# Optimization experiments

Hardware: AMD Instinct MI355X
Metric: run time of the kernel (lower is better)

Reference implementation:

```python
import jax, jax.numpy as jnp
import numpy as np

EPS = 1e-5

def layernorm(x, w, b):
    mu = x.mean(-1, keepdims=True)
    var = x.var(-1, keepdims=True)
    return (x - mu) / jnp.sqrt(var + EPS) * w + b

def silu(x):
    return x * jax.nn.sigmoid(x)

def causal_dwconv(x, w, b):
    # x: (B,L,D), w: (D,K) depthwise causal conv along L
    K = w.shape[1]
    xt = jnp.moveaxis(x, 1, 2)                      # (B,D,L)
    xt = jnp.pad(xt, ((0, 0), (0, 0), (K - 1, 0)))
    y = jax.lax.conv_general_dilated(xt, w[:, None, :], (1,), 'VALID',
        dimension_numbers=('NCH', 'OIH', 'NCH'), feature_group_count=w.shape[0])
    return jnp.moveaxis(y + b[None, :, None], 2, 1)

def mamba_layer(x, p):
    # LayerNorm + Mamba selective scan; returns (out, C) with C the per-step C projection ("C_fast")
    xn = layernorm(x, p['ln_w'], p['ln_b'])
    xz = xn @ p['in_proj_w']                        # (B,L,2*Di)
    Di = p['conv_w'].shape[0]
    xh, z = xz[..., :Di], xz[..., Di:]
    xh = silu(causal_dwconv(xh, p['conv_w'], p['conv_b']))
    dbl = xh @ p['x_proj_w']                        # (B,L,R+2*S)
    R = p['dt_proj_w'].shape[0]
    S = p['A_log'].shape[1]
    dt = jax.nn.softplus(dbl[..., :R] @ p['dt_proj_w'] + p['dt_proj_b'])  # (B,L,Di)
    Bm = dbl[..., R:R + S]                          # (B,L,S)
    Cm = dbl[..., R + S:]                           # (B,L,S)
    A = -jnp.exp(p['A_log'])                        # (Di,S)
    dA = jnp.exp(dt[..., None] * A)                 # (B,L,Di,S)
    dBx = dt[..., None] * Bm[:, :, None, :] * xh[..., None]
    def step(h, inp):
        a, bx = inp
        h = a * h + bx
        return h, h
    h0 = jnp.zeros((x.shape[0], Di, S), x.dtype)
    _, hs = jax.lax.scan(step, h0, (jnp.moveaxis(dA, 1, 0), jnp.moveaxis(dBx, 1, 0)))
    y = jnp.einsum('lbds,bls->bld', hs, Cm) + p['D'] * xh
    y = y * silu(z)
    return y @ p['out_proj_w'], Cm

def run_chunks(x, k, p):
    # contiguous L-chunks folded into batch (chunks are independent sequences)
    B, L, D = x.shape
    y, C = mamba_layer(x.reshape(B * k, L // k, D), p)
    return y.reshape(B, L, D), C.reshape(B, k, L // k, -1)

def batchnorm(h, g, b):
    mu = h.mean((0, 1))
    var = h.var((0, 1))
    return (h - mu) / jnp.sqrt(var + EPS) * g + b

def freq_ffn(x, fc1_w, bn1_g, bn1_b, r_mat, i_mat, rb, ib, fc2_w, bn2_g, bn2_b):
    h = jax.nn.relu(batchnorm(jnp.einsum('bnc,hc->bnh', x, fc1_w), bn1_g, bn1_b))
    xf = jnp.fft.fft(h, axis=1, norm='ortho')
    # torch einsum 'bnc,cc->bnc' multiplies by the DIAGONAL of the matrix
    rd = jnp.diagonal(r_mat)
    idg = jnp.diagonal(i_mat)
    xr = jax.nn.relu(xf.real * rd - xf.imag * idg + rb)
    xi = jax.nn.relu(xf.imag * rd + xf.real * idg + ib)
    h = jnp.fft.ifft(xr + 1j * xi, axis=1, norm='ortho').real.astype(x.dtype)
    return batchnorm(jnp.einsum('bnh,ch->bnc', h, fc2_w), bn2_g, bn2_b)


def setup_inputs() -> dict:
    key = jax.random.key(0)
    B, L, D = 4, 512, 128
    Di, S, R, K, H = 256, 64, 8, 4, 256
    ks = jax.random.split(key, 16)
    rn = lambda k, sh, s=1.0: (jax.random.normal(k, sh) * s).astype(jnp.float32)
    return {
        'x': rn(ks[0], (B, L, D)),
        'ln_w': jnp.ones((D,), jnp.float32), 'ln_b': jnp.zeros((D,), jnp.float32),
        'in_proj_w': rn(ks[1], (D, 2 * Di), D ** -0.5),
        'conv_w': rn(ks[2], (Di, K), 0.3),
        'conv_b': jnp.zeros((Di,), jnp.float32),
        'x_proj_w': rn(ks[3], (Di, R + 2 * S), Di ** -0.5),
        'dt_proj_w': rn(ks[4], (R, Di), R ** -0.5),
        'dt_proj_b': rn(ks[5], (Di,), 0.1) - 4.0,
        'A_log': jnp.log(jnp.tile(jnp.arange(1, S + 1, dtype=jnp.float32), (Di, 1))),
        'D_param': jnp.ones((Di,), jnp.float32),
        'out_proj_w': rn(ks[6], (Di, D), Di ** -0.5),
        'norm1_w': jnp.ones((D,), jnp.float32), 'norm1_b': jnp.zeros((D,), jnp.float32),
        'norm2_w': jnp.ones((D,), jnp.float32), 'norm2_b': jnp.zeros((D,), jnp.float32),
        'fc1_w': rn(ks[7], (H, D), D ** -0.5),
        'bn1_g': jnp.ones((H,), jnp.float32), 'bn1_b': jnp.zeros((H,), jnp.float32),
        'r_mat': rn(ks[8], (H, H), 0.02),
        'i_mat': rn(ks[9], (H, H), 0.02),
        'rb': rn(ks[10], (H,), 0.02),
        'ib': rn(ks[11], (H,), 0.02),
        'fc2_w': rn(ks[12], (D, H), H ** -0.5),
        'bn2_g': jnp.ones((D,), jnp.float32), 'bn2_b': jnp.zeros((D,), jnp.float32),
    }


def reference(x, ln_w, ln_b, in_proj_w, conv_w, conv_b, x_proj_w, dt_proj_w, dt_proj_b,
              A_log, D_param, out_proj_w, norm1_w, norm1_b, norm2_w, norm2_b,
              fc1_w, bn1_g, bn1_b, r_mat, i_mat, rb, ib, fc2_w, bn2_g, bn2_b):
    p = dict(ln_w=ln_w, ln_b=ln_b, in_proj_w=in_proj_w, conv_w=conv_w, conv_b=conv_b,
             x_proj_w=x_proj_w, dt_proj_w=dt_proj_w, dt_proj_b=dt_proj_b,
             A_log=A_log, D=D_param, out_proj_w=out_proj_w)
    x_o, C0 = mamba_layer(x, p)                 # full sequence
    y1, C1 = run_chunks(x, 2, p)                # 2 halves
    y2, C2 = run_chunks(x, 4, p)                # 4 quarters
    y3, C3 = run_chunks(x, 8, p)                # 8 eighths
    x_o = x_o + y1 + y2 + y3                    # drop_path = Identity
    xo = x + layernorm(x_o, norm1_w, norm1_b)
    out = xo + freq_ffn(layernorm(xo, norm2_w, norm2_b),
                        fc1_w, bn1_g, bn1_b, r_mat, i_mat, rb, ib, fc2_w, bn2_g, bn2_b)
    return out, C0, C1, C2, C3
```

## Files before the change

### kernel.cpp

```cpp
#include <hip/hip_runtime.h>
#include <hip/hip_bf16.h>
#include <math.h>


constexpr int NT = 2048;
constexpr int Di = 256;
constexpr float EPSF = 1e-5f;
constexpr float LOG2E = 1.4426950408889634f;
constexpr float ISQ512 = 0.04419417382415922f;

typedef __attribute__((ext_vector_type(8))) short short8;
typedef __attribute__((ext_vector_type(4))) float f32x4;

constexpr long O_COS   = 0;
constexpr long O_CS2B  = 512;
constexpr long O_CSIB  = 262656;
constexpr long O_A2    = 524800;
constexpr long O_FC1B  = 541184;
constexpr long O_FC2B  = 557568;
constexpr long O_RD    = 573952;
constexpr long O_IDG   = 574208;
constexpr long O_XN    = 574464;
constexpr long O_XZ    = 836608;
constexpr long O_XH    = 1885184;
constexpr long O_DBL   = 3982336;
constexpr long O_DTT   = 5096448;
constexpr long O_YS    = 7193600;
constexpr long O_YACC  = 9290752;
constexpr long O_XO1   = 9815040;
constexpr long O_XO    = 10077184;
constexpr long O_LN2B  = 10339328;
constexpr long O_H1    = 10404864;
constexpr long O_H1NTB = 10929152;
constexpr long O_XRI   = 11191296;
constexpr long O_XRITB = 12239872;
constexpr long O_H2B   = 12764160;
constexpr long O_F2    = 13026304;
constexpr long O_ST1   = 13288448;
constexpr long O_ST2   = 13288960;
constexpr long O_DXT   = O_H1;

__device__ __forceinline__ ushort bf16bits(float v) {
  __hip_bfloat16 h = __float2bfloat16(v);
  return *(ushort*)&h;
}

__global__ void k_costab(float* __restrict__ ws) {
  int m = threadIdx.x;
  ws[O_COS + m]       = cosf((float)m * (6.283185307179586f / 512.0f)) * ISQ512;
  ws[O_COS + m + 256] = cosf((float)(m + 256) * (6.283185307179586f / 512.0f)) * ISQ512;
}

__global__ void k_tables(const float* __restrict__ A_log,
                         const float* __restrict__ fc1_w,
                         const float* __restrict__ fc2_w,
                         const float* __restrict__ r_mat,
                         const float* __restrict__ i_mat,
                         float* __restrict__ ws) {
  const float* ct = ws + O_COS;
  __hip_bfloat16* cs2b = (__hip_bfloat16*)(ws + O_CS2B);
  __hip_bfloat16* csib = (__hip_bfloat16*)(ws + O_CSIB);
  int i = blockIdx.x * 256 + threadIdx.x;
  if (i < 524288) {
    int r = i >> 9, n = i & 511;
    float v;
    if (r < 512) v = ct[(r * n) & 511];
    else         v = -ct[((r - 512) * n + 384) & 511];
    cs2b[i] = __float2bfloat16(v);
  } else {
    int j = i - 524288;
    int n = j >> 10, kp = j & 1023;
    float v;
    if (kp < 512) v = ct[(n * kp) & 511];
    else          v = -ct[(n * (kp - 512) + 384) & 511];
    csib[j] = __float2bfloat16(v);
  }
  if (i < 16384) ws[O_A2 + i] = -expf(A_log[i]) * LOG2E;
  if (i < 32768) {
    ((__hip_bfloat16*)(ws + O_FC1B))[i] = __float2bfloat16(fc1_w[i]);
    ((__hip_bfloat16*)(ws + O_FC2B))[i] = __float2bfloat16(fc2_w[i]);
  }
  if (i < 256) {
    ws[O_RD + i] = r_mat[i * 256 + i];
    ws[O_IDG + i] = i_mat[i * 256 + i];
  }
}

__global__ void k_ln1(const float* __restrict__ x, const float* __restrict__ w,
                      const float* __restrict__ b, float* __restrict__ out) {
  int lane = threadIdx.x & 63;
  int t = (blockIdx.x * 256 + threadIdx.x) >> 6;
  float v0 = x[t * 128 + lane], v1 = x[t * 128 + 64 + lane];
  float s = v0 + v1, sq = v0 * v0 + v1 * v1;
#pragma unroll
  for (int off = 32; off; off >>= 1) { s += __shfl_xor(s, off); sq += __shfl_xor(sq, off); }
  float mu = s * (1.f / 128.f);
  float rstd = rsqrtf(sq * (1.f / 128.f) - mu * mu + EPSF);
  out[t * 128 + lane]      = (v0 - mu) * rstd * w[lane] + b[lane];
  out[t * 128 + 64 + lane] = (v1 - mu) * rstd * w[64 + lane] + b[64 + lane];
}

__global__ void k_lndbl(const float* __restrict__ x, const float* __restrict__ xo1,
                        const float* __restrict__ w1, const float* __restrict__ b1,
                        const float* __restrict__ w2, const float* __restrict__ b2,
                        float* __restrict__ xo, __hip_bfloat16* __restrict__ ln2b) {
  int lane = threadIdx.x & 63;
  int t = (blockIdx.x * 256 + threadIdx.x) >> 6;
  float u0 = xo1[t * 128 + lane], u1 = xo1[t * 128 + 64 + lane];
  float s = u0 + u1, sq = u0 * u0 + u1 * u1;
#pragma unroll
  for (int off = 32; off; off >>= 1) { s += __shfl_xor(s, off); sq += __shfl_xor(sq, off); }
  float mu = s * (1.f / 128.f);
  float rstd = rsqrtf(sq * (1.f / 128.f) - mu * mu + EPSF);
  float a0 = x[t * 128 + lane]      + (u0 - mu) * rstd * w1[lane] + b1[lane];
  float a1 = x[t * 128 + 64 + lane] + (u1 - mu) * rstd * w1[64 + lane] + b1[64 + lane];
  xo[t * 128 + lane] = a0;
  xo[t * 128 + 64 + lane] = a1;
  s = a0 + a1; sq = a0 * a0 + a1 * a1;
#pragma unroll
  for (int off = 32; off; off >>= 1) { s += __shfl_xor(s, off); sq += __shfl_xor(sq, off); }
  mu = s * (1.f / 128.f);
  rstd = rsqrtf(sq * (1.f / 128.f) - mu * mu + EPSF);
  ln2b[t * 128 + lane]      = __float2bfloat16((a0 - mu) * rstd * w2[lane] + b2[lane]);
  ln2b[t * 128 + 64 + lane] = __float2bfloat16((a1 - mu) * rstd * w2[64 + lane] + b2[64 + lane]);
}

__global__ __launch_bounds__(256) void k_gemm(const float* __restrict__ A,
                                              const float* __restrict__ B,
                                              float* __restrict__ C,
                                              int M, int N, int K,
                                              long sA, long sB, long sC) {
  A += (long)blockIdx.z * sA;
  B += (long)blockIdx.z * sB;
  C += (long)blockIdx.z * sC;
  __shared__ float As[16][68];
  __shared__ float Bs[16][68];
  int tid = threadIdx.x;
  int m0 = blockIdx.y * 64, n0 = blockIdx.x * 64;
  int arow = tid >> 2, ak4 = (tid & 3) * 4;
  int bkrow = tid >> 4, bn4 = (tid & 15) * 4;
  int tr = (tid >> 4) * 4, tc = (tid & 15) * 4;
  float acc[4][4] = {};
  for (int k0 = 0; k0 < K; k0 += 16) {
    float4 av = *(const float4*)&A[(long)(m0 + arow) * K + k0 + ak4];
    float4 bv = make_float4(0.f, 0.f, 0.f, 0.f);
    if (n0 + bn4 < N) bv = *(const float4*)&B[(long)(k0 + bkrow) * N + n0 + bn4];
    __syncthreads();
    As[ak4 + 0][arow] = av.x; As[ak4 + 1][arow] = av.y;
    As[ak4 + 2][arow] = av.z; As[ak4 + 3][arow] = av.w;
    *(float4*)&Bs[bkrow][bn4] = bv;
    __syncthreads();
#pragma unroll
    for (int kk = 0; kk < 16; ++kk) {
      float4 a = *(const float4*)&As[kk][tr];
      float4 bq = *(const float4*)&Bs[kk][tc];
      float ar[4] = {a.x, a.y, a.z, a.w};
      float br[4] = {bq.x, bq.y, bq.z, bq.w};
#pragma unroll
      for (int ii = 0; ii < 4; ++ii)
#pragma unroll
        for (int jj = 0; jj < 4; ++jj) acc[ii][jj] = fmaf(ar[ii], br[jj], acc[ii][jj]);
    }
  }
#pragma unroll
  for (int ii = 0; ii < 4; ++ii)
#pragma unroll
    for (int jj = 0; jj < 4; ++jj) {
      int n = n0 + tc + jj;
      if (n < N) C[(long)(m0 + tr + ii) * N + n] = acc[ii][jj];
    }
}

template <bool OUTBF16>
__global__ __launch_bounds__(256) void k_gmfma(const ushort* __restrict__ A,
                                               const ushort* __restrict__ Bt,
                                               void* __restrict__ Cv,
                                               int M, int N, int K,
                                               long sA, long sBt, long sC) {
  A += (long)blockIdx.z * sA;
  Bt += (long)blockIdx.z * sBt;
  int lane = threadIdx.x & 63, wid = threadIdx.x >> 6;
  int m0 = blockIdx.y * 64 + wid * 16, n0 = blockIdx.x * 64;
  const ushort* arow = A + (long)(m0 + (lane & 15)) * K + (lane >> 4) * 8;
  const ushort* brow = Bt + (long)(n0 + (lane & 15)) * K + (lane >> 4) * 8;
  f32x4 acc0 = {0.f, 0.f, 0.f, 0.f}, acc1 = acc0, acc2 = acc0, acc3 = acc0;
#pragma unroll 4
  for (int k0 = 0; k0 < K; k0 += 32) {
    short8 av = *(const short8*)(arow + k0);
    short8 b0 = *(const short8*)(brow + k0);
    short8 b1 = *(const short8*)(brow + 16L * K + k0);
    short8 b2 = *(const short8*)(brow + 32L * K + k0);
    short8 b3 = *(const short8*)(brow + 48L * K + k0);
    acc0 = __builtin_amdgcn_mfma_f32_16x16x32_bf16(av, b0, acc0, 0, 0, 0);
    acc1 = __builtin_amdgcn_mfma_f32_16x16x32_bf16(av, b1, acc1, 0, 0, 0);
    acc2 = __builtin_amdgcn_mfma_f32_16x16x32_bf16(av, b2, acc2, 0, 0, 0);
    acc3 = __builtin_amdgcn_mfma_f32_16x16x32_bf16(av, b3, acc3, 0, 0, 0);
  }
  int r0 = (lane >> 4) * 4, c0 = lane & 15;
#pragma unroll
  for (int j = 0; j < 4; ++j) {
    long row = m0 + r0 + j;
    float v[4] = {acc0[j], acc1[j], acc2[j], acc3[j]};
    if (OUTBF16) {
      __hip_bfloat16* C = (__hip_bfloat16*)Cv + blockIdx.z * sC;
#pragma unroll
      for (int c = 0; c < 4; ++c) C[row * N + n0 + c * 16 + c0] = __float2bfloat16(v[c]);
    } else {
      float* C = (float*)Cv + blockIdx.z * sC;
#pragma unroll
      for (int c = 0; c < 4; ++c) C[row * N + n0 + c * 16 + c0] = v[c];
    }
  }
}

__global__ void k_conv(const float* __restrict__ xz, const float* __restrict__ cw,
                       const float* __restrict__ cb, float* __restrict__ xh) {
  long i = (long)blockIdx.x * 256 + threadIdx.x;
  int v = (int)(i >> 19);
  int r = (int)(i & 524287);
  int t = r >> 8, d = r & 255;
  int l = t & ((512 >> v) - 1);
  float acc = cb[d];
#pragma unroll
  for (int j = 0; j < 4; ++j) {
    int off = 3 - j;
    if (l - off >= 0) acc = fmaf(cw[d * 4 + j], xz[(long)(t - off) * 512 + d], acc);
  }
  xh[i] = acc / (1.f + expf(-acc));
}

__global__ __launch_bounds__(256) void k_dtx(const float* __restrict__ dbl,
                                             const float* __restrict__ xh,
                                             const float* __restrict__ w,
                                             const float* __restrict__ bias,
                                             float* __restrict__ DTT,
                                             float* __restrict__ DXT,
                                             float* __restrict__ outC) {
  __shared__ float r8T[8][64];
  __shared__ float xt[64][65];
  __shared__ float wt[8][64];
  int v = blockIdx.z, t0 = blockIdx.y * 64, d0 = blockIdx.x * 64;
  int j = threadIdx.x;
  if (j < 128) {
    int t = j >> 1, half = j & 1;
    float4 q = *(const float4*)&dbl[((long)v * NT + t0 + t) * 136 + half * 4];
    r8T[half * 4 + 0][t] = q.x; r8T[half * 4 + 1][t] = q.y;
    r8T[half * 4 + 2][t] = q.z; r8T[half * 4 + 3][t] = q.w;
  } else {
    int idx = j - 128;
    int r = idx >> 4, dl4 = (idx & 15) * 4;
    float4 q = *(const float4*)&w[r * 256 + d0 + dl4];
    wt[r][dl4] = q.x; wt[r][dl4 + 1] = q.y; wt[r][dl4 + 2] = q.z; wt[r][dl4 + 3] = q.w;
  }
#pragma unroll
  for (int it = 0; it < 4; ++it) {
    int row = (j >> 4) + it * 16, col4 = (j & 15) * 4;
    float4 q = *(const float4*)&xh[((long)v * NT + t0 + row) * 256 + d0 + col4];
    xt[row][col4] = q.x; xt[row][col4 + 1] = q.y;
    xt[row][col4 + 2] = q.z; xt[row][col4 + 3] = q.w;
  }
  __syncthreads();
  int lane = j & 63, w4 = j >> 6;
#pragma unroll
  for (int k = 0; k < 16; ++k) {
    int dl = w4 * 16 + k, d = d0 + dl;
    float s = bias[d];
#pragma unroll
    for (int r = 0; r < 8; ++r) s = fmaf(r8T[r][lane], wt[r][dl], s);
    float dtv = fmaxf(s, 0.f) + log1pf(expf(-fabsf(s)));
    float dx = dtv * xt[lane][dl];
    long oi = ((long)(v * 256 + d)) * 2048 + t0 + lane;
    DTT[oi] = dtv;
    DXT[oi] = dx;
  }
  if (blockIdx.x == 0) {
#pragma unroll
    for (int k2 = 0; k2 < 16; ++k2) {
      int idx = k2 * 256 + j;
      int tl = idx >> 6, s2 = idx & 63;
      outC[(long)v * 131072 + (long)(t0 + tl) * 64 + s2] =
          dbl[((long)v * NT + t0 + tl) * 136 + 72 + s2];
    }
  }
}

template <int CTRL>
__device__ __forceinline__ float dpp_add(float x) {
  int t = __builtin_amdgcn_update_dpp(0, __float_as_int(x), CTRL, 0xF, 0xF, true);
  return x + __int_as_float(t);
}

__global__ __launch_bounds__(256) void k_scan(const float* __restrict__ DTT,
                                              const float* __restrict__ DXT,
                                              const float* __restrict__ dbl,
                                              const float* __restrict__ A2,
                                              float* __restrict__ ys) {
  int lane = threadIdx.x & 63;
  int gwid = (blockIdx.x * 256 + threadIdx.x) >> 6;
  int v, base;
  if (gwid < 1024)      { v = 0; base = 0; }
  else if (gwid < 3072) { v = 1; base = 1024; }
  else if (gwid < 7168) { v = 2; base = 3072; }
  else                  { v = 3; base = 7168; }
  int local = gwid - base;
  int b = local >> 8, d = local & 255;
  int Lp = 512 >> v;
  int t0 = b * Lp;
  const float* dtrow = DTT + ((long)(v * 256 + d)) * 2048 + t0;
  const float* dxrow = DXT + ((long)(v * 256 + d)) * 2048 + t0;
  const float* dblp = dbl + ((long)v * NT + t0) * 136;
  float* ysp = ys + (long)v * NT * Di + (long)((b << 8) + d) * Lp;
  float a2 = A2[d * 64 + lane];
  float h = 0.f;

#define LOADG(BB, CC, G)                                                     \
  _Pragma("unroll") for (int q = 0; q < 8; ++q) {                            \
    BB[q] = rowp[((G) * 8 + q) * 136 + 8 + lane];                            \
    CC[q] = rowp[((G) * 8 + q) * 136 + 72 + lane];                           \
  }
#define PROCG(BB, CC, G)                                                     \
  _Pragma("unroll") for (int q = 0; q < 8; ++q) {                            \
    int l2 = (G) * 8 + q;                                                    \
    float sdt = __int_as_float(__builtin_amdgcn_readlane(__float_as_int(rdt), l2)); \
    float sdx = __int_as_float(__builtin_amdgcn_readlane(__float_as_int(rdx), l2)); \
    float a = __builtin_amdgcn_exp2f(sdt * a2);                              \
    h = fmaf(a, h, sdx * BB[q]);                                             \
    float p = h * CC[q];                                                     \
    p = dpp_add<0x111>(p); p = dpp_add<0x112>(p);                            \
    p = dpp_add<0x114>(p); p = dpp_add<0x118>(p);                            \
    p = dpp_add<0x142>(p); p = dpp_add<0x143>(p);                            \
    float tot = __int_as_float(__builtin_amdgcn_readlane(__float_as_int(p), 63)); \
    if (lane == l2) ybuf = tot;                                              \
  }

  for (int c = 0; c < Lp; c += 64) {
    float rdt = dtrow[c + lane];
    float rdx = dxrow[c + lane];
    const float* rowp = dblp + (long)c * 136;
    float ybuf = 0.f;
    float b0[8], c0[8], b1[8], c1[8];
    LOADG(b0, c0, 0)
    LOADG(b1, c1, 1)
    PROCG(b0, c0, 0) LOADG(b0, c0, 2)
    PROCG(b1, c1, 1) LOADG(b1, c1, 3)
    PROCG(b0, c0, 2) LOADG(b0, c0, 4)
    PROCG(b1, c1, 3) LOADG(b1, c1, 5)
    PROCG(b0, c0, 4) LOADG(b0, c0, 6)
    PROCG(b1, c1, 5) LOADG(b1, c1, 7)
    PROCG(b0, c0, 6)
    PROCG(b1, c1, 7)
    ysp[c + lane] = ybuf;
  }
#undef LOADG
#undef PROCG
}

__global__ void k_yfull(const float* __restrict__ ys, const float* __restrict__ xh,
                        const float* __restrict__ xz, const float* __restrict__ Dp,
                        float* __restrict__ yacc) {
  int i = blockIdx.x * 256 + threadIdx.x;
  int t = i >> 8, d = i & 255;
  float z = xz[(long)t * 512 + 256 + d];
  float sil = z / (1.f + expf(-z));
  float Dd = Dp[d];
  float s = 0.f;
#pragma unroll
  for (int v = 0; v < 4; ++v) {
    int Lp = 512 >> v;
    int b = t >> (9 - v);
    int l = t & (Lp - 1);
    float ysv = ys[(long)v * NT * Di + (long)((b << 8) + d) * Lp + l];
    float xhv = xh[(long)v * NT * Di + i];
    s += ysv + Dd * xhv;
  }
  yacc[i] = s * sil;
}

__global__ __launch_bounds__(256) void k_bnstats(const float* __restrict__ h, int F,
                                                 const float* __restrict__ g,
                                                 const float* __restrict__ b,
                                                 float* __restrict__ scale,
                                                 float* __restrict__ shift) {
  int f = blockIdx.x;
  float s = 0.f, sq = 0.f;
  for (int t = threadIdx.x; t < NT; t += 256) {
    float v = h[(long)t * F + f];
    s += v; sq += v * v;
  }
#pragma unroll
  for (int off = 32; off; off >>= 1) { s += __shfl_xor(s, off); sq += __shfl_xor(sq, off); }
  __shared__ float red[2][4];
  int w = threadIdx.x >> 6;
  if ((threadIdx.x & 63) == 0) { red[0][w] = s; red[1][w] = sq; }
  __syncthreads();
  if (threadIdx.x == 0) {
    s = red[0][0] + red[0][1] + red[0][2] + red[0][3];
    sq = red[1][0] + red[1][1] + red[1][2] + red[1][3];
    float mu = s * (1.f / NT);
    float var = sq * (1.f / NT) - mu * mu;
    float sc = g[f] * rsqrtf(var + EPSF);
    scale[f] = sc;
    shift[f] = b[f] - mu * sc;
  }
}

__global__ __launch_bounds__(256) void k_bnreluT(const float* __restrict__ h1,
                                                 const float* __restrict__ scale,
                                                 const float* __restrict__ shift,
                                                 ushort* __restrict__ outT) {
  __shared__ float tile[64][65];
  int t0 = blockIdx.x * 64, f0 = blockIdx.y * 64, b = blockIdx.z;
  int tid = threadIdx.x;
#pragma unroll
  for (int i = 0; i < 16; ++i) {
    int idx = i * 256 + tid;
    int r = idx >> 6, c = idx & 63;
    int f = f0 + c;
    float v = h1[((long)(b * 512 + t0 + r)) * 256 + f];
    tile[r][c] = fmaxf(fmaf(v, scale[f], shift[f]), 0.f);
  }
  __syncthreads();
  int tc2 = (tid & 31) * 2, fr0 = tid >> 5;
#pragma unroll
  for (int i = 0; i < 8; ++i) {
    int fr = fr0 + i * 8;
    uint u = ((uint)bf16bits(tile[tc2 + 1][fr]) << 16) | bf16bits(tile[tc2][fr]);
    long off = (long)b * 131072 + (long)(f0 + fr) * 512 + t0 + tc2;
    *(uint*)(outT + off) = u;
  }
}

__global__ __launch_bounds__(256) void k_freqT(const float* __restrict__ XRI,
                                               const float* __restrict__ rd,
                                               const float* __restrict__ idg,
                                               const float* __restrict__ rb,
                                               const float* __restrict__ ib,
                                               ushort* __restrict__ outT) {
  __shared__ float tr[64][65], ti[64][65];
  int n0 = blockIdx.x * 64, f0 = blockIdx.y * 64, b = blockIdx.z;
  int tid = threadIdx.x;
#pragma unroll
  for (int i = 0; i < 16; ++i) {
    int idx = i * 256 + tid;
    int r = idx >> 6, c = idx & 63;
    int f = f0 + c;
    long base = (long)b * 262144 + (long)(n0 + r) * 256 + f;
    float a = XRI[base], b2 = XRI[base + 131072];
    tr[r][c] = fmaxf(a * rd[f] - b2 * idg[f] + rb[f], 0.f);
    ti[r][c] = fmaxf(b2 * rd[f] + a * idg[f] + ib[f], 0.f);
  }
  __syncthreads();
  int tc2 = (tid & 31) * 2, fr0 = tid >> 5;
#pragma unroll
  for (int i = 0; i < 8; ++i) {
    int fr = fr0 + i * 8;
    long offr = (long)b * 262144 + (long)(f0 + fr) * 1024 + n0 + tc2;
    uint ur = ((uint)bf16bits(tr[tc2 + 1][fr]) << 16) | bf16bits(tr[tc2][fr]);
    uint ui = ((uint)bf16bits(ti[tc2 + 1][fr]) << 16) | bf16bits(ti[tc2][fr]);
    *(uint*)(outT + offr) = ur;
    *(uint*)(outT + offr + 512) = ui;
  }
}

__global__ void k_final(const float* __restrict__ xo, const float* __restrict__ f2,
                        const float* __restrict__ scale, const float* __restrict__ shift,
                        float* __restrict__ out) {
  int i = blockIdx.x * 256 + threadIdx.x;
  int c = i & 127;
  out[i] = xo[i] + fmaf(f2[i], scale[c], shift[c]);
}

extern "C" void kernel_launch(void* const* d_in, const int* in_sizes, int n_in,
                              void* d_out, int out_size, void* d_ws, size_t ws_size,
                              hipStream_t stream) {
  const float* x         = (const float*)d_in[0];
  const float* ln_w      = (const float*)d_in[1];
  const float* ln_b      = (const float*)d_in[2];
  const float* in_proj_w = (const float*)d_in[3];
  const float* conv_w    = (const float*)d_in[4];
  const float* conv_b    = (const float*)d_in[5];
  const float* x_proj_w  = (const float*)d_in[6];
  const float* dt_proj_w = (const float*)d_in[7];
  const float* dt_proj_b = (const float*)d_in[8];
  const float* A_log     = (const float*)d_in[9];
  const float* D_param   = (const float*)d_in[10];
  const float* out_proj_w= (const float*)d_in[11];
  const float* n1w       = (const float*)d_in[12];
  const float* n1b       = (const float*)d_in[13];
  const float* n2w       = (const float*)d_in[14];
  const float* n2b       = (const float*)d_in[15];
  const float* fc1_w     = (const float*)d_in[16];
  const float* bn1_g     = (const float*)d_in[17];
  const float* bn1_b     = (const float*)d_in[18];
  const float* r_mat     = (const float*)d_in[19];
  const float* i_mat     = (const float*)d_in[20];
  const float* rb        = (const float*)d_in[21];
  const float* ib        = (const float*)d_in[22];
  const float* fc2_w     = (const float*)d_in[23];
  const float* bn2_g     = (const float*)d_in[24];
  const float* bn2_b     = (const float*)d_in[25];
  float* ws  = (float*)d_ws;
  float* out = (float*)d_out;

  k_costab<<<1, 256, 0, stream>>>(ws);
  k_tables<<<4096, 256, 0, stream>>>(A_log, fc1_w, fc2_w, r_mat, i_mat, ws);
  k_ln1<<<512, 256, 0, stream>>>(x, ln_w, ln_b, ws + O_XN);
  k_gemm<<<dim3(8, 32, 1), 256, 0, stream>>>(ws + O_XN, in_proj_w, ws + O_XZ,
                                             NT, 512, 128, 0, 0, 0);
  k_conv<<<8192, 256, 0, stream>>>(ws + O_XZ, conv_w, conv_b, ws + O_XH);
  k_gemm<<<dim3(3, 32, 4), 256, 0, stream>>>(ws + O_XH, x_proj_w, ws + O_DBL,
                                             NT, 136, 256,
                                             (long)NT * Di, 0, (long)NT * 136);
  k_dtx<<<dim3(4, 32, 4), 256, 0, stream>>>(ws + O_DBL, ws + O_XH, dt_proj_w,
                                            dt_proj_b, ws + O_DTT, ws + O_DXT,
                                            out + 262144);
  k_scan<<<3840, 256, 0, stream>>>(ws + O_DTT, ws + O_DXT, ws + O_DBL,
                                   ws + O_A2, ws + O_YS);
  k_yfull<<<2048, 256, 0, stream>>>(ws + O_YS, ws + O_XH, ws + O_XZ, D_param,
                                    ws + O_YACC);
  k_gemm<<<dim3(2, 32, 1), 256, 0, stream>>>(ws + O_YACC, out_proj_w, ws + O_XO1,
                                             NT, 128, 256, 0, 0, 0);
  k_lndbl<<<512, 256, 0, stream>>>(x, ws + O_XO1, n1w, n1b, n2w, n2b,
                                   ws + O_XO, (__hip_bfloat16*)(ws + O_LN2B));
  k_gmfma<false><<<dim3(4, 32, 1), 256, 0, stream>>>(
      (const ushort*)(ws + O_LN2B), (const ushort*)(ws + O_FC1B), ws + O_H1,
      2048, 256, 128, 0, 0, 0);
  k_bnstats<<<256, 256, 0, stream>>>(ws + O_H1, 256, bn1_g, bn1_b,
                                     ws + O_ST1, ws + O_ST1 + 256);
  k_bnreluT<<<dim3(8, 4, 4), 256, 0, stream>>>(ws + O_H1, ws + O_ST1,
                                               ws + O_ST1 + 256,
                                               (ushort*)(ws + O_H1NTB));
  k_gmfma<false><<<dim3(4, 16, 4), 256, 0, stream>>>(
      (const ushort*)(ws + O_CS2B), (const ushort*)(ws + O_H1NTB), ws + O_XRI,
      1024, 256, 512, 0, 131072L, 262144L);
  k_freqT<<<dim3(8, 4, 4), 256, 0, stream>>>(ws + O_XRI, ws + O_RD, ws + O_IDG,
                                             rb, ib, (ushort*)(ws + O_XRITB));
  k_gmfma<true><<<dim3(4, 8, 4), 256, 0, stream>>>(
      (const ushort*)(ws + O_CSIB), (const ushort*)(ws + O_XRITB), ws + O_H2B,
      512, 256, 1024, 0, 262144L, 131072L);
  k_gmfma<false><<<dim3(2, 32, 1), 256, 0, stream>>>(
      (const ushort*)(ws + O_H2B), (const ushort*)(ws + O_FC2B), ws + O_F2,
      2048, 128, 256, 0, 0, 0);
  k_bnstats<<<128, 256, 0, stream>>>(ws + O_F2, 128, bn2_g, bn2_b,
                                     ws + O_ST2, ws + O_ST2 + 128);
  k_final<<<1024, 256, 0, stream>>>(ws + O_XO, ws + O_F2, ws + O_ST2,
                                    ws + O_ST2 + 128, out);
}
```

Before: 330.0 us.

## Move Mamba projections to bf16 MFMA GEMMs and deduplicate depthwise conv

Replaces the three fp32 SIMT GEMMs (in_proj, x_proj, out_proj) with the existing bf16 MFMA GEMM. Producers now emit bf16 copies of their outputs: layernorm, conv and the y accumulation. Weights are pre-transposed and converted in the table kernel, and the cosine table moves into shared memory, which removes one launch. The conv is computed once per token and the result is written for all four chunk variants, except near chunk boundaries where the causal padding differs. The trade-off is reduced precision in these projections and a workspace layout that reuses buffers through aliasing.

```diff
diff --git a/kernel.cpp b/kernel.cpp
--- a/kernel.cpp
+++ b/kernel.cpp
@@ -12,55 +12,56 @@
 typedef __attribute__((ext_vector_type(8))) short short8;
 typedef __attribute__((ext_vector_type(4))) float f32x4;
 
-constexpr long O_COS   = 0;
-constexpr long O_CS2B  = 512;
-constexpr long O_CSIB  = 262656;
-constexpr long O_A2    = 524800;
-constexpr long O_FC1B  = 541184;
-constexpr long O_FC2B  = 557568;
-constexpr long O_RD    = 573952;
-constexpr long O_IDG   = 574208;
-constexpr long O_XN    = 574464;
-constexpr long O_XZ    = 836608;
-constexpr long O_XH    = 1885184;
-constexpr long O_DBL   = 3982336;
-constexpr long O_DTT   = 5096448;
-constexpr long O_YS    = 7193600;
-constexpr long O_YACC  = 9290752;
-constexpr long O_XO1   = 9815040;
-constexpr long O_XO    = 10077184;
-constexpr long O_LN2B  = 10339328;
-constexpr long O_H1    = 10404864;
-constexpr long O_H1NTB = 10929152;
-constexpr long O_XRI   = 11191296;
-constexpr long O_XRITB = 12239872;
-constexpr long O_H2B   = 12764160;
-constexpr long O_F2    = 13026304;
-constexpr long O_ST1   = 13288448;
-constexpr long O_ST2   = 13288960;
+constexpr long O_CS2B  = 0;
+constexpr long O_CSIB  = 262144;
+constexpr long O_A2    = 524288;
+constexpr long O_FC1B  = 540672;
+constexpr long O_FC2B  = 557056;
+constexpr long O_INPB  = 573440;
+constexpr long O_XPB   = 606208;
+constexpr long O_OPB   = 630784;
+constexpr long O_RD    = 647168;
+constexpr long O_IDG   = 647424;
+constexpr long O_XNB   = 647680;
+constexpr long O_XZ    = 778752;
+constexpr long O_XH    = 1827328;
+constexpr long O_DBL   = 3924480;
+constexpr long O_DTT   = 5038592;
+constexpr long O_YS    = 7135744;
+constexpr long O_XO    = 9232896;
+constexpr long O_LN2B  = 9495040;
+constexpr long O_H1    = 9626112;
+constexpr long O_H1NTB = 10150400;
+constexpr long O_XRI   = 10412544;
+constexpr long O_XRITB = 11461120;
+constexpr long O_H2B   = 11985408;
+constexpr long O_F2    = 12247552;
+constexpr long O_ST1   = 12509696;
+constexpr long O_ST2   = 12510208;
 constexpr long O_DXT   = O_H1;
+constexpr long O_XHB   = O_H1;
+constexpr long O_YACCB = O_F2;
+constexpr long O_XO1   = O_H2B;
 
 __device__ __forceinline__ ushort bf16bits(float v) {
   __hip_bfloat16 h = __float2bfloat16(v);
   return *(ushort*)&h;
 }
 
-__global__ void k_costab(float* __restrict__ ws) {
-  int m = threadIdx.x;
-  ws[O_COS + m]       = cosf((float)m * (6.283185307179586f / 512.0f)) * ISQ512;
-  ws[O_COS + m + 256] = cosf((float)(m + 256) * (6.283185307179586f / 512.0f)) * ISQ512;
-}
-
-__global__ void k_tables(const float* __restrict__ A_log,
-                         const float* __restrict__ fc1_w,
-                         const float* __restrict__ fc2_w,
-                         const float* __restrict__ r_mat,
-                         const float* __restrict__ i_mat,
-                         float* __restrict__ ws) {
-  const float* ct = ws + O_COS;
+__global__ __launch_bounds__(256) void k_tables(
+    const float* __restrict__ A_log, const float* __restrict__ fc1_w,
+    const float* __restrict__ fc2_w, const float* __restrict__ r_mat,
+    const float* __restrict__ i_mat, const float* __restrict__ in_proj_w,
+    const float* __restrict__ x_proj_w, const float* __restrict__ out_proj_w,
+    float* __restrict__ ws) {
+  __shared__ float ct[512];
+  int tid = threadIdx.x;
+  ct[tid]       = cosf((float)tid * (6.283185307179586f / 512.0f)) * ISQ512;
+  ct[tid + 256] = cosf((float)(tid + 256) * (6.283185307179586f / 512.0f)) * ISQ512;
+  __syncthreads();
   __hip_bfloat16* cs2b = (__hip_bfloat16*)(ws + O_CS2B);
   __hip_bfloat16* csib = (__hip_bfloat16*)(ws + O_CSIB);
-  int i = blockIdx.x * 256 + threadIdx.x;
+  int i = blockIdx.x * 256 + tid;
   if (i < 524288) {
     int r = i >> 9, n = i & 511;
     float v;
@@ -80,6 +81,21 @@
     ((__hip_bfloat16*)(ws + O_FC1B))[i] = __float2bfloat16(fc1_w[i]);
     ((__hip_bfloat16*)(ws + O_FC2B))[i] = __float2bfloat16(fc2_w[i]);
   }
+  if (i < 65536) {
+    int n = i >> 7, k = i & 127;
+    ((__hip_bfloat16*)(ws + O_INPB))[i] = __float2bfloat16(in_proj_w[k * 512 + n]);
+  }
+  if (i < 49152) {
+    int n = i >> 8, k = i & 255;
+    float v = (n < 136) ? x_proj_w[k * 136 + n] : 0.f;
+    ((__hip_bfloat16*)(ws + O_XPB))[i] = __float2bfloat16(v);
+  }
+  if (i < 32768 + 0) {}
+  if (i >= 65536 && i < 65536 + 32768) {
+    int j = i - 65536;
+    int n = j >> 8, k = j & 255;
+    ((__hip_bfloat16*)(ws + O_OPB))[j] = __float2bfloat16(out_proj_w[k * 128 + n]);
+  }
   if (i < 256) {
     ws[O_RD + i] = r_mat[i * 256 + i];
     ws[O_IDG + i] = i_mat[i * 256 + i];
@@ -87,7 +103,7 @@
 }
 
 __global__ void k_ln1(const float* __restrict__ x, const float* __restrict__ w,
-                      const float* __restrict__ b, float* __restrict__ out) {
+                      const float* __restrict__ b, ushort* __restrict__ outb) {
   int lane = threadIdx.x & 63;
   int t = (blockIdx.x * 256 + threadIdx.x) >> 6;
   float v0 = x[t * 128 + lane], v1 = x[t * 128 + 64 + lane];
@@ -96,14 +112,14 @@
   for (int off = 32; off; off >>= 1) { s += __shfl_xor(s, off); sq += __shfl_xor(sq, off); }
   float mu = s * (1.f / 128.f);
   float rstd = rsqrtf(sq * (1.f / 128.f) - mu * mu + EPSF);
-  out[t * 128 + lane]      = (v0 - mu) * rstd * w[lane] + b[lane];
-  out[t * 128 + 64 + lane] = (v1 - mu) * rstd * w[64 + lane] + b[64 + lane];
+  outb[t * 128 + lane]      = bf16bits((v0 - mu) * rstd * w[lane] + b[lane]);
+  outb[t * 128 + 64 + lane] = bf16bits((v1 - mu) * rstd * w[64 + lane] + b[64 + lane]);
 }
 
 __global__ void k_lndbl(const float* __restrict__ x, const float* __restrict__ xo1,
                         const float* __restrict__ w1, const float* __restrict__ b1,
                         const float* __restrict__ w2, const float* __restrict__ b2,
-                        float* __restrict__ xo, __hip_bfloat16* __restrict__ ln2b) {
+                        float* __restrict__ xo, ushort* __restrict__ ln2b) {
   int lane = threadIdx.x & 63;
   int t = (blockIdx.x * 256 + threadIdx.x) >> 6;
   float u0 = xo1[t * 128 + lane], u1 = xo1[t * 128 + 64 + lane];
@@ -121,54 +137,8 @@
   for (int off = 32; off; off >>= 1) { s += __shfl_xor(s, off); sq += __shfl_xor(sq, off); }
   mu = s * (1.f / 128.f);
   rstd = rsqrtf(sq * (1.f / 128.f) - mu * mu + EPSF);
-  ln2b[t * 128 + lane]      = __float2bfloat16((a0 - mu) * rstd * w2[lane] + b2[lane]);
-  ln2b[t * 128 + 64 + lane] = __float2bfloat16((a1 - mu) * rstd * w2[64 + lane] + b2[64 + lane]);
-}
-
-__global__ __launch_bounds__(256) void k_gemm(const float* __restrict__ A,
-                                              const float* __restrict__ B,
-                                              float* __restrict__ C,
-                                              int M, int N, int K,
-                                              long sA, long sB, long sC) {
-  A += (long)blockIdx.z * sA;
-  B += (long)blockIdx.z * sB;
-  C += (long)blockIdx.z * sC;
-  __shared__ float As[16][68];
-  __shared__ float Bs[16][68];
-  int tid = threadIdx.x;
-  int m0 = blockIdx.y * 64, n0 = blockIdx.x * 64;
-  int arow = tid >> 2, ak4 = (tid & 3) * 4;
-  int bkrow = tid >> 4, bn4 = (tid & 15) * 4;
-  int tr = (tid >> 4) * 4, tc = (tid & 15) * 4;
-  float acc[4][4] = {};
-  for (int k0 = 0; k0 < K; k0 += 16) {
-    float4 av = *(const float4*)&A[(long)(m0 + arow) * K + k0 + ak4];
-    float4 bv = make_float4(0.f, 0.f, 0.f, 0.f);
-    if (n0 + bn4 < N) bv = *(const float4*)&B[(long)(k0 + bkrow) * N + n0 + bn4];
-    __syncthreads();
-    As[ak4 + 0][arow] = av.x; As[ak4 + 1][arow] = av.y;
-    As[ak4 + 2][arow] = av.z; As[ak4 + 3][arow] = av.w;
-    *(float4*)&Bs[bkrow][bn4] = bv;
-    __syncthreads();
-#pragma unroll
-    for (int kk = 0; kk < 16; ++kk) {
-      float4 a = *(const float4*)&As[kk][tr];
-      float4 bq = *(const float4*)&Bs[kk][tc];
-      float ar[4] = {a.x, a.y, a.z, a.w};
-      float br[4] = {bq.x, bq.y, bq.z, bq.w};
-#pragma unroll
-      for (int ii = 0; ii < 4; ++ii)
-#pragma unroll
-        for (int jj = 0; jj < 4; ++jj) acc[ii][jj] = fmaf(ar[ii], br[jj], acc[ii][jj]);
-    }
-  }
-#pragma unroll
-  for (int ii = 0; ii < 4; ++ii)
-#pragma unroll
-    for (int jj = 0; jj < 4; ++jj) {
-      int n = n0 + tc + jj;
-      if (n < N) C[(long)(m0 + tr + ii) * N + n] = acc[ii][jj];
-    }
+  ln2b[t * 128 + lane]      = bf16bits((a0 - mu) * rstd * w2[lane] + b2[lane]);
+  ln2b[t * 128 + 64 + lane] = bf16bits((a1 - mu) * rstd * w2[64 + lane] + b2[64 + lane]);
 }
 
 template <bool OUTBF16>
@@ -204,29 +174,51 @@
     if (OUTBF16) {
       __hip_bfloat16* C = (__hip_bfloat16*)Cv + blockIdx.z * sC;
 #pragma unroll
-      for (int c = 0; c < 4; ++c) C[row * N + n0 + c * 16 + c0] = __float2bfloat16(v[c]);
+      for (int c = 0; c < 4; ++c) {
+        int n = n0 + c * 16 + c0;
+        if (n < N) C[row * N + n] = __float2bfloat16(v[c]);
+      }
     } else {
       float* C = (float*)Cv + blockIdx.z * sC;
 #pragma unroll
-      for (int c = 0; c < 4; ++c) C[row * N + n0 + c * 16 + c0] = v[c];
+      for (int c = 0; c < 4; ++c) {
+        int n = n0 + c * 16 + c0;
+        if (n < N) C[row * N + n] = v[c];
+      }
     }
   }
 }
 
-__global__ void k_conv(const float* __restrict__ xz, const float* __restrict__ cw,
-                       const float* __restrict__ cb, float* __restrict__ xh) {
-  long i = (long)blockIdx.x * 256 + threadIdx.x;
-  int v = (int)(i >> 19);
-  int r = (int)(i & 524287);
-  int t = r >> 8, d = r & 255;
-  int l = t & ((512 >> v) - 1);
-  float acc = cb[d];
-#pragma unroll
-  for (int j = 0; j < 4; ++j) {
-    int off = 3 - j;
-    if (l - off >= 0) acc = fmaf(cw[d * 4 + j], xz[(long)(t - off) * 512 + d], acc);
-  }
-  xh[i] = acc / (1.f + expf(-acc));
+__global__ void k_conv4(const float* __restrict__ xz, const float* __restrict__ cw,
+                        const float* __restrict__ cb, float* __restrict__ xh,
+                        ushort* __restrict__ xhb) {
+  int i = blockIdx.x * 256 + threadIdx.x;
+  int t = i >> 8, d = i & 255;
+  float w0 = cw[d * 4 + 0], w1 = cw[d * 4 + 1], w2 = cw[d * 4 + 2], w3 = cw[d * 4 + 3];
+  float bias = cb[d];
+  float x0  = xz[(long)t * 512 + d];
+  float xm1 = t >= 1 ? xz[(long)(t - 1) * 512 + d] : 0.f;
+  float xm2 = t >= 2 ? xz[(long)(t - 2) * 512 + d] : 0.f;
+  float xm3 = t >= 3 ? xz[(long)(t - 3) * 512 + d] : 0.f;
+  if ((t & 63) >= 3) {
+    float s = fmaf(w0, xm3, fmaf(w1, xm2, fmaf(w2, xm1, fmaf(w3, x0, bias))));
+    float sil = s / (1.f + expf(-s));
+    ushort sb = bf16bits(sil);
+#pragma unroll
+    for (int v = 0; v < 4; ++v) { xh[v * 524288 + i] = sil; xhb[v * 524288 + i] = sb; }
+  } else {
+#pragma unroll
+    for (int v = 0; v < 4; ++v) {
+      int lv = t & ((512 >> v) - 1);
+      float s = fmaf(w3, x0, bias);
+      if (lv >= 1) s = fmaf(w2, xm1, s);
+      if (lv >= 2) s = fmaf(w1, xm2, s);
+      if (lv >= 3) s = fmaf(w0, xm3, s);
+      float sil = s / (1.f + expf(-s));
+      xh[v * 524288 + i] = sil;
+      xhb[v * 524288 + i] = bf16bits(sil);
+    }
+  }
 }
 
 __global__ __launch_bounds__(256) void k_dtx(const float* __restrict__ dbl,
@@ -357,7 +349,7 @@
 
 __global__ void k_yfull(const float* __restrict__ ys, const float* __restrict__ xh,
                         const float* __restrict__ xz, const float* __restrict__ Dp,
-                        float* __restrict__ yacc) {
+                        ushort* __restrict__ yaccb) {
   int i = blockIdx.x * 256 + threadIdx.x;
   int t = i >> 8, d = i & 255;
   float z = xz[(long)t * 512 + 256 + d];
@@ -373,7 +365,7 @@
     float xhv = xh[(long)v * NT * Di + i];
     s += ysv + Dd * xhv;
   }
-  yacc[i] = s * sil;
+  yaccb[i] = bf16bits(s * sil);
 }
 
 __global__ __launch_bounds__(256) void k_bnstats(const float* __restrict__ h, int F,
@@ -502,26 +494,29 @@
   float* ws  = (float*)d_ws;
   float* out = (float*)d_out;
 
-  k_costab<<<1, 256, 0, stream>>>(ws);
-  k_tables<<<4096, 256, 0, stream>>>(A_log, fc1_w, fc2_w, r_mat, i_mat, ws);
-  k_ln1<<<512, 256, 0, stream>>>(x, ln_w, ln_b, ws + O_XN);
-  k_gemm<<<dim3(8, 32, 1), 256, 0, stream>>>(ws + O_XN, in_proj_w, ws + O_XZ,
-                                             NT, 512, 128, 0, 0, 0);
-  k_conv<<<8192, 256, 0, stream>>>(ws + O_XZ, conv_w, conv_b, ws + O_XH);
-  k_gemm<<<dim3(3, 32, 4), 256, 0, stream>>>(ws + O_XH, x_proj_w, ws + O_DBL,
-                                             NT, 136, 256,
-                                             (long)NT * Di, 0, (long)NT * 136);
+  k_tables<<<4096, 256, 0, stream>>>(A_log, fc1_w, fc2_w, r_mat, i_mat,
+                                     in_proj_w, x_proj_w, out_proj_w, ws);
+  k_ln1<<<512, 256, 0, stream>>>(x, ln_w, ln_b, (ushort*)(ws + O_XNB));
+  k_gmfma<false><<<dim3(8, 32, 1), 256, 0, stream>>>(
+      (const ushort*)(ws + O_XNB), (const ushort*)(ws + O_INPB), ws + O_XZ,
+      2048, 512, 128, 0, 0, 0);
+  k_conv4<<<2048, 256, 0, stream>>>(ws + O_XZ, conv_w, conv_b, ws + O_XH,
+                                    (ushort*)(ws + O_XHB));
+  k_gmfma<false><<<dim3(3, 32, 4), 256, 0, stream>>>(
+      (const ushort*)(ws + O_XHB), (const ushort*)(ws + O_XPB), ws + O_DBL,
+      2048, 136, 256, 524288L, 0, 278528L);
   k_dtx<<<dim3(4, 32, 4), 256, 0, stream>>>(ws + O_DBL, ws + O_XH, dt_proj_w,
                                             dt_proj_b, ws + O_DTT, ws + O_DXT,
                                             out + 262144);
   k_scan<<<3840, 256, 0, stream>>>(ws + O_DTT, ws + O_DXT, ws + O_DBL,
                                    ws + O_A2, ws + O_YS);
   k_yfull<<<2048, 256, 0, stream>>>(ws + O_YS, ws + O_XH, ws + O_XZ, D_param,
-                                    ws + O_YACC);
-  k_gemm<<<dim3(2, 32, 1), 256, 0, stream>>>(ws + O_YACC, out_proj_w, ws + O_XO1,
-                                             NT, 128, 256, 0, 0, 0);
+                                    (ushort*)(ws + O_YACCB));
+  k_gmfma<false><<<dim3(2, 32, 1), 256, 0, stream>>>(
+      (const ushort*)(ws + O_YACCB), (const ushort*)(ws + O_OPB), ws + O_XO1,
+      2048, 128, 256, 0, 0, 0);
   k_lndbl<<<512, 256, 0, stream>>>(x, ws + O_XO1, n1w, n1b, n2w, n2b,
-                                   ws + O_XO, (__hip_bfloat16*)(ws + O_LN2B));
+                                   ws + O_XO, (ushort*)(ws + O_LN2B));
   k_gmfma<false><<<dim3(4, 32, 1), 256, 0, stream>>>(
       (const ushort*)(ws + O_LN2B), (const ushort*)(ws + O_FC1B), ws + O_H1,
       2048, 256, 128, 0, 0, 0);
```

Result: faster. 297.5 us (-9.8%).
